# Kernel optimization log

Measured on AMD Instinct MI355X. Metric: run time of the kernel, lower is better.

Reference implementation:

```python
import jax, jax.numpy as jnp
import numpy as np

N, DF, DR, H, K = 4096, 128, 64, 1024, 10


def _init_linear(key, fan_in, fan_out):
    kw, kb = jax.random.split(key)
    bound = 1.0 / np.sqrt(fan_in)
    W = jax.random.uniform(kw, (fan_in, fan_out), jnp.float32, -bound, bound)
    b = jax.random.uniform(kb, (fan_out,), jnp.float32, -bound, bound)
    return W, b


def setup_inputs() -> dict:
    key = jax.random.key(0)
    ks = jax.random.split(key, 8)
    condition = jax.random.normal(ks[0], (N, DF), jnp.float32)
    tensor = jax.random.normal(ks[1], (N, DR), jnp.float32)
    Win, b_in = _init_linear(ks[2], DF + DR, H)
    W1, b1 = _init_linear(ks[3], H, H)
    W2, b2 = _init_linear(ks[4], H, H)
    W3, b3 = _init_linear(ks[5], H, H)
    Wout, b_out = _init_linear(ks[6], H, DR)
    return {"condition": condition, "tensor": tensor,
            "Win": Win, "b_in": b_in, "W1": W1, "b1": b1,
            "W2": W2, "b2": b2, "W3": W3, "b3": b3,
            "Wout": Wout, "b_out": b_out}


def _mlp(x, Win, b_in, W1, b1, W2, b2, W3, b3, Wout, b_out):
    # FFNN: input layer + 3 hidden layers with Softplus, linear output -> DR
    h = jax.nn.softplus(x @ Win + b_in)
    h = jax.nn.softplus(h @ W1 + b1)
    h = jax.nn.softplus(h @ W2 + b2)
    h = jax.nn.softplus(h @ W3 + b3)
    return h @ Wout + b_out


def reference(condition, tensor, Win, b_in, W1, b1, W2, b2, W3, b3, Wout, b_out):
    # torch.cdist(condition, condition), p=2 -> [N, N]
    sq = jnp.sum(condition * condition, axis=-1)
    d2 = sq[:, None] + sq[None, :] - 2.0 * (condition @ condition.T)
    dist = jnp.sqrt(jnp.maximum(d2, 0.0))
    # torch.topk(dist, 10, dim=1, largest=False) -> k nearest neighbor indices
    _, neighbor_idx = jax.lax.top_k(-dist, K)  # [N, K]
    # gather neighbor groups
    cond_g = condition[neighbor_idx]  # [N, K, DF]
    tens_g = tensor[neighbor_idx]     # [N, K, DR]
    # MongeMapNetwork.pushforward: tensor - MLP(concat(condition, tensor))
    x = jnp.concatenate([cond_g, tens_g], axis=-1)  # [N, K, DF+DR]
    pushed = tens_g - _mlp(x, Win, b_in, W1, b1, W2, b2, W3, b3, Wout, b_out)
    return pushed  # [N, K, DR]
```

## Files before the change

kernel.cpp:

```cpp
#include <hip/hip_runtime.h>
#include <hip/hip_fp16.h>
#include <stdint.h>

typedef unsigned short u16;
typedef unsigned int   u32;
typedef unsigned long long u64;
typedef short v8bf __attribute__((ext_vector_type(8)));
typedef float v4f  __attribute__((ext_vector_type(4)));
typedef u16   v8u  __attribute__((ext_vector_type(8)));

#define NPTS 4096
#define DF   128
#define DR   64
#define HID  1024
#define KNN  10
#define DIN  192

#define AS1 __attribute__((address_space(1)))
#define AS3 __attribute__((address_space(3)))

__device__ __forceinline__ float bf2f(u16 b){ return __uint_as_float(((unsigned)b)<<16); }
__device__ __forceinline__ u16 f2bf(float f){
  unsigned u = __float_as_uint(f);
  unsigned r = 0x7fffu + ((u>>16)&1u);
  return (u16)((u + r)>>16);
}
__device__ __forceinline__ u16 f2h(float f){
  __half h = __float2half(f);
  return __half_as_ushort(h);
}
__device__ __forceinline__ float softplus_f(float x){
  return x>15.f ? x : __logf(1.f + __expf(x));
}
__device__ __forceinline__ float rdv(const void* p, long j, int fl){
  return fl ? bf2f(((const u16*)p)[j]) : ((const float*)p)[j];
}
__device__ __forceinline__ void gl2lds16(const u16* g, u16* l){
  __builtin_amdgcn_global_load_lds((const AS1 unsigned int*)g, (AS3 unsigned int*)l, 16, 0, 0);
}

__global__ void detect_k(const u16* __restrict__ c, int* __restrict__ flag){
  __shared__ int cnt[256];
  int t = threadIdx.x, n = 0;
  for(int i=t; i<8192; i+=256){
    u16 v = c[2*i];
    int e = (v>>7)&0xff;
    n += (e>=96 && e<=158);
  }
  cnt[t] = n; __syncthreads();
  for(int s=128; s>0; s>>=1){ if(t<s) cnt[t]+=cnt[t+s]; __syncthreads(); }
  if(t==0) *flag = (cnt[0] > 4915) ? 1 : 0;
}

__global__ void prep_k(const void* cond, const void* tens,
    const void* Wi, const void* W1, const void* W2, const void* W3, const void* Wo,
    const void* bi, const void* b1, const void* b2, const void* b3, const void* bo,
    float* __restrict__ condF, float* __restrict__ tensF, float* __restrict__ biasF,
    u16* Oi, u16* O1, u16* O2, u16* O3, u16* Oo,
    float* __restrict__ sq, u16* __restrict__ X, const int* __restrict__ flag){
  __shared__ u16 tile[32][33];
  const int fl = *flag;
  const int bid = blockIdx.x, tid = threadIdx.x;
  if(bid < 3089){
    int i = bid*256 + tid;
    if(i < 524288){ condF[i] = rdv(cond, i, fl); }
    else if(i < 786432){ tensF[i-524288] = rdv(tens, i-524288, fl); }
    else{
      int j = i - 786432;
      if(j < 1024)      biasF[j] = rdv(bi, j, fl);
      else if(j < 2048) biasF[j] = rdv(b1, j-1024, fl);
      else if(j < 3072) biasF[j] = rdv(b2, j-2048, fl);
      else if(j < 4096) biasF[j] = rdv(b3, j-3072, fl);
      else if(j < 4160) biasF[j] = rdv(bo, j-4096, fl);
    }
  } else if(bid < 6417){
    int b = bid - 3089;
    const void* in; u16* out; int R, C, bx, by;
    if(b < 192)      {              in=Wi; out=Oi; R=192;  C=1024; bx=b&31; by=b>>5; }
    else if(b < 1216){ b -= 192;    in=W1; out=O1; R=1024; C=1024; bx=b&31; by=b>>5; }
    else if(b < 2240){ b -= 1216;   in=W2; out=O2; R=1024; C=1024; bx=b&31; by=b>>5; }
    else if(b < 3264){ b -= 2240;   in=W3; out=O3; R=1024; C=1024; bx=b&31; by=b>>5; }
    else             { b -= 3264;   in=Wo; out=Oo; R=1024; C=64;   bx=b&1;  by=b>>1; }
    int gx = bx*32, gy = by*32;
    int tx = tid&31, ty = tid>>5;
    #pragma unroll
    for(int r=ty; r<32; r+=8){
      size_t idx = (size_t)(gy+r)*C + gx + tx;
      tile[r][tx] = fl ? ((const u16*)in)[idx] : f2bf(((const float*)in)[idx]);
    }
    __syncthreads();
    #pragma unroll
    for(int r=ty; r<32; r+=8) out[(size_t)(gx+r)*R + gy + tx] = tile[tx][r];
  } else if(bid < 7441){
    int b = bid - 6417;
    int row = b*4 + (tid>>6), lane = tid&63;
    float a = rdv(cond, (long)row*DF + lane, fl);
    float c2 = rdv(cond, (long)row*DF + lane + 64, fl);
    double s = (double)a*a + (double)c2*c2;
    #pragma unroll
    for(int off=32; off>0; off>>=1) s += __shfl_down(s, off, 64);
    if(lane==0) sq[row] = (float)s;
  } else {
    int c = (bid-7441)*256 + tid;
    int j = c/48;
    int off = (c - j*48)*4;
    ushort4 o;
    if(off < DF){
      o.x = f2bf(rdv(cond, (long)j*DF + off + 0, fl));
      o.y = f2bf(rdv(cond, (long)j*DF + off + 1, fl));
      o.z = f2bf(rdv(cond, (long)j*DF + off + 2, fl));
      o.w = f2bf(rdv(cond, (long)j*DF + off + 3, fl));
    }else{
      int t2 = off - DF;
      o.x = f2bf(rdv(tens, (long)j*DR + t2 + 0, fl));
      o.y = f2bf(rdv(tens, (long)j*DR + t2 + 1, fl));
      o.z = f2bf(rdv(tens, (long)j*DR + t2 + 2, fl));
      o.w = f2bf(rdv(tens, (long)j*DR + t2 + 3, fl));
    }
    *(ushort4*)&X[(size_t)j*DIN + off] = o;
  }
}

__device__ __forceinline__ void gemm128_body(const u16* __restrict__ A,
    const u16* __restrict__ Bt, const float* __restrict__ bias, u16* __restrict__ C,
    int Kc, int bid, u16* As, u16* Bs){
  const int wg = (bid&7)*32 + (bid>>3);
  const int bm = (wg>>3)*128, bn = (wg&7)*128;
  const int lane = threadIdx.x&63, wave = threadIdx.x>>6;
  const int wm = (wave&1)*64, wn = (wave>>1)*64;
  const int sr = wave*32 + (lane>>2), sc = (lane&3)*8;
  const u16* pA0 = A  + (size_t)(bm+sr   )*Kc + sc;
  const u16* pA1 = A  + (size_t)(bm+sr+16)*Kc + sc;
  const u16* pB0 = Bt + (size_t)(bn+sr   )*Kc + sc;
  const u16* pB1 = Bt + (size_t)(bn+sr+16)*Kc + sc;
  u16* lA0 = &As[wave*1024];
  u16* lA1 = &As[wave*1024 + 512];
  u16* lB0 = &Bs[wave*1024];
  u16* lB1 = &Bs[wave*1024 + 512];
  const int m16 = lane&15, q = lane>>4;
  v4f acc[4][4] = {};
  for(int kb=0; kb<Kc; kb+=32){
    gl2lds16(pA0 + kb, lA0);
    gl2lds16(pA1 + kb, lA1);
    gl2lds16(pB0 + kb, lB0);
    gl2lds16(pB1 + kb, lB1);
    __syncthreads();
    v8bf a[4], b[4];
    #pragma unroll
    for(int x=0;x<4;x++){
      a[x] = *(const v8bf*)&As[(wm + x*16 + m16)*32 + q*8];
      b[x] = *(const v8bf*)&Bs[(wn + x*16 + m16)*32 + q*8];
    }
    #pragma unroll
    for(int mi=0;mi<4;mi++)
      #pragma unroll
      for(int ni=0;ni<4;ni++)
        acc[mi][ni] = __builtin_amdgcn_mfma_f32_16x16x32_bf16(a[mi], b[ni], acc[mi][ni], 0,0,0);
    __syncthreads();
  }
  const int col16 = lane&15, rowq = lane>>4;
  #pragma unroll
  for(int mi=0;mi<4;mi++){
    #pragma unroll
    for(int ni=0;ni<4;ni++){
      int cn = bn + wn + ni*16 + col16;
      float bi = bias[cn];
      #pragma unroll
      for(int r=0;r<4;r++){
        int rw = bm + wm + mi*16 + rowq*4 + r;
        float v = softplus_f(acc[mi][ni][r] + bi);
        C[(size_t)rw*HID + cn] = f2bf(v);
      }
    }
  }
}

__device__ __forceinline__ void knn_body(const u16* __restrict__ distH,
    const float* __restrict__ condF, int* __restrict__ nidx, int row,
    float* __restrict__ af, int* __restrict__ scnt,
    int* __restrict__ cand, u64* __restrict__ keys){
  const int lane = threadIdx.x&63;
  af[lane]    = condF[(size_t)row*DF + lane];
  af[lane+64] = condF[(size_t)row*DF + lane + 64];
  if(lane==0) *scnt = 0;
  const v8u* drow = (const v8u*)(distH + (size_t)row*NPTS);
  v8u vals[8];
  #pragma unroll
  for(int k=0;k<8;k++) vals[k] = drow[lane + k*64];
  u32 mx = 0;
  #pragma unroll
  for(int k=0;k<8;k++)
    #pragma unroll
    for(int e=0;e<8;e++){ u32 v = vals[k][e]; mx = v>mx ? v : mx; }
  #pragma unroll
  for(int off=32; off>0; off>>=1){
    u32 o = (u32)__shfl_down((int)mx, off, 64); mx = o>mx ? o : mx;
  }
  mx = (u32)__shfl((int)mx, 0, 64);
  u32 hi = mx+1, lo = 0;
  for(int it=0; it<17; ++it){
    u32 mid = (lo+hi)>>1;
    int c = 0;
    #pragma unroll
    for(int k=0;k<8;k++)
      #pragma unroll
      for(int e=0;e<8;e++) c += ((u32)vals[k][e] < mid);
    #pragma unroll
    for(int off=32; off>0; off>>=1) c += __shfl_down(c, off, 64);
    c = __shfl(c, 0, 64);
    if(c >= 16){ hi = mid; if(c <= 48) break; }
    else lo = mid;
  }
  const u32 t = hi;
  #pragma unroll
  for(int k=0;k<8;k++)
    #pragma unroll
    for(int e=0;e<8;e++){
      if((u32)vals[k][e] < t){
        int s = atomicAdd(scnt, 1);
        if(s < 64) cand[s] = (lane + k*64)*8 + e;
      }
    }
  int cnt = *scnt; if(cnt > 64) cnt = 64;
  u64 mykey = ~0ULL; int myj = -1;
  if(lane < cnt){
    int j = cand[lane];
    const float4* bp4 = (const float4*)(condF + (size_t)j*DF);
    double s = 0.0;
    #pragma unroll
    for(int v4i=0; v4i<32; v4i++){
      float4 bv = bp4[v4i];
      double d0 = (double)af[v4i*4+0]-(double)bv.x;
      double d1 = (double)af[v4i*4+1]-(double)bv.y;
      double d2 = (double)af[v4i*4+2]-(double)bv.z;
      double d3 = (double)af[v4i*4+3]-(double)bv.w;
      s += d0*d0 + d1*d1 + d2*d2 + d3*d3;
    }
    u64 bits = (u64)__double_as_longlong(s);
    mykey = (bits & ~0xFFFULL) | (u32)j;
    myj = j;
  }
  keys[lane] = mykey;
  if(lane < cnt){
    int rank = 0;
    for(int c2=0;c2<cnt;c2++) rank += (keys[c2] < mykey);
    if(rank < KNN) nidx[row*KNN + rank] = myj;
  }
}

__global__ __launch_bounds__(256,2) void gram_g1_k(const u16* __restrict__ condB,
    const float* __restrict__ condF, const float* __restrict__ sq,
    u16* __restrict__ distH, const int* __restrict__ flag,
    const u16* __restrict__ X, const u16* __restrict__ Wt_in,
    const float* __restrict__ biasF, u16* __restrict__ A0){
  __shared__ __align__(16) u16 smem[20480];
  const int bid = blockIdx.x;
  if(bid < 256){
    gemm128_body(X, Wt_in, biasF, A0, DIN, bid, smem, smem+4096);
    return;
  }
  const int gb = bid - 256;
  u16* Ahi = smem;
  u16* Alo = smem + 5120;
  u16* Bhi = smem + 10240;
  u16* Blo = smem + 15360;
  const int fl = *flag;
  const int bm = (gb&31)*128, bn = (gb>>5)*128;
  const int tid = threadIdx.x, lane = tid&63, wave = tid>>6;
  const int wm = (wave&1)*64, wn = (wave>>1)*64;
  v4f acc[4][4] = {};
  for(int kb=0; kb<DF; kb+=32){
    if(fl){
      #pragma unroll
      for(int t=0;t<2;t++){
        int c2 = tid + t*256;
        int r = c2>>2, col = (c2&3)*8;
        *(uint4*)&Ahi[r*40+col] = *(const uint4*)&condB[(size_t)(bm+r)*DF + kb + col];
        *(uint4*)&Bhi[r*40+col] = *(const uint4*)&condB[(size_t)(bn+r)*DF + kb + col];
      }
    }else{
      #pragma unroll
      for(int t=0;t<4;t++){
        int ch = tid + t*256;
        int r = ch>>3, c = (ch&7)*4;
        float4 av = *(const float4*)&condF[(size_t)(bm+r)*DF + kb + c];
        float4 bv = *(const float4*)&condF[(size_t)(bn+r)*DF + kb + c];
        ushort4 ah, bh, al, bl;
        ah.x=f2bf(av.x); ah.y=f2bf(av.y); ah.z=f2bf(av.z); ah.w=f2bf(av.w);
        bh.x=f2bf(bv.x); bh.y=f2bf(bv.y); bh.z=f2bf(bv.z); bh.w=f2bf(bv.w);
        al.x=f2bf(av.x-bf2f(ah.x)); al.y=f2bf(av.y-bf2f(ah.y));
        al.z=f2bf(av.z-bf2f(ah.z)); al.w=f2bf(av.w-bf2f(ah.w));
        bl.x=f2bf(bv.x-bf2f(bh.x)); bl.y=f2bf(bv.y-bf2f(bh.y));
        bl.z=f2bf(bv.z-bf2f(bh.z)); bl.w=f2bf(bv.w-bf2f(bh.w));
        *(ushort4*)&Ahi[r*40+c] = ah; *(ushort4*)&Bhi[r*40+c] = bh;
        *(ushort4*)&Alo[r*40+c] = al; *(ushort4*)&Blo[r*40+c] = bl;
      }
    }
    __syncthreads();
    const int m16 = lane&15, q = lane>>4;
    v8bf ahf[4], bhf[4];
    #pragma unroll
    for(int x=0;x<4;x++){
      ahf[x] = *(const v8bf*)&Ahi[(wm + x*16 + m16)*40 + q*8];
      bhf[x] = *(const v8bf*)&Bhi[(wn + x*16 + m16)*40 + q*8];
    }
    if(!fl){
      v8bf alf[4], blf[4];
      #pragma unroll
      for(int x=0;x<4;x++){
        alf[x] = *(const v8bf*)&Alo[(wm + x*16 + m16)*40 + q*8];
        blf[x] = *(const v8bf*)&Blo[(wn + x*16 + m16)*40 + q*8];
      }
      #pragma unroll
      for(int mi=0;mi<4;mi++)
        #pragma unroll
        for(int ni=0;ni<4;ni++){
          acc[mi][ni] = __builtin_amdgcn_mfma_f32_16x16x32_bf16(alf[mi], bhf[ni], acc[mi][ni], 0,0,0);
          acc[mi][ni] = __builtin_amdgcn_mfma_f32_16x16x32_bf16(ahf[mi], blf[ni], acc[mi][ni], 0,0,0);
        }
    }
    #pragma unroll
    for(int mi=0;mi<4;mi++)
      #pragma unroll
      for(int ni=0;ni<4;ni++)
        acc[mi][ni] = __builtin_amdgcn_mfma_f32_16x16x32_bf16(ahf[mi], bhf[ni], acc[mi][ni], 0,0,0);
    __syncthreads();
  }
  const int col16 = lane&15, rowq = lane>>4;
  #pragma unroll
  for(int mi=0;mi<4;mi++){
    #pragma unroll
    for(int ni=0;ni<4;ni++){
      int cj = bn + wn + ni*16 + col16;
      float sqj = sq[cj];
      #pragma unroll
      for(int r=0;r<4;r++){
        int ri = bm + wm + mi*16 + rowq*4 + r;
        float d2 = (sq[ri] + sqj) - 2.0f*acc[mi][ni][r];
        distH[(size_t)ri*NPTS + cj] = f2h(fmaxf(d2, 0.f));
      }
    }
  }
}

__global__ __launch_bounds__(256,2) void gemm_knn_k(const u16* __restrict__ A,
    const u16* __restrict__ Bt, const float* __restrict__ bias, u16* __restrict__ C,
    const u16* __restrict__ distH, const float* __restrict__ condF,
    int* __restrict__ nidx, int rowoff){
  __shared__ __align__(16) u16 gsm[8192];
  __shared__ float af[4][DF];
  __shared__ int   scnt[4];
  __shared__ int   cand[4][64];
  __shared__ u64   keys[4][64];
  const int bid = blockIdx.x;
  if(bid < 256){
    gemm128_body(A, Bt, bias, C, HID, bid, gsm, gsm+4096);
  } else {
    const int wv = threadIdx.x>>6;
    const int row = rowoff + (bid-256)*4 + wv;
    knn_body(distH, condF, nidx, row, af[wv], &scnt[wv], cand[wv], keys[wv]);
  }
}

__global__ __launch_bounds__(256,2) void gemm_bt_k(const u16* __restrict__ A,
    const u16* __restrict__ Bt, const float* __restrict__ bias, u16* __restrict__ C){
  __shared__ __align__(16) u16 As[4096];
  __shared__ __align__(16) u16 Bs[4096];
  gemm128_body(A, Bt, bias, C, HID, blockIdx.x, As, Bs);
}

__global__ __launch_bounds__(256,2) void gemm_out_k(const u16* __restrict__ A,
    const u16* __restrict__ Bt, float* __restrict__ Pp){
  __shared__ __align__(16) u16 As[128*32];
  __shared__ __align__(16) u16 Bs[64*32];
  const int bm = (blockIdx.x>>2)*128;
  const int k0 = (blockIdx.x&3)*256;
  float* P = Pp + (size_t)(blockIdx.x&3)*262144;
  const int tid = threadIdx.x, lane = tid&63, wave = tid>>6;
  const int wm = wave*32;
  int c0 = wave*128 + lane, c1 = c0 + 64;
  int ra0 = c0>>2, qa0 = c0&3, ra1 = c1>>2, qa1 = c1&3;
  int cb = wave*64 + lane;
  int rb = cb>>2, qb = cb&3;
  const u16* pA0 = A  + (size_t)(bm+ra0)*HID + qa0*8;
  const u16* pA1 = A  + (size_t)(bm+ra1)*HID + qa1*8;
  const u16* pB  = Bt + (size_t)rb*HID + qb*8;
  u16* lA0 = &As[(wave*128     )*8];
  u16* lA1 = &As[(wave*128 + 64)*8];
  u16* lB  = &Bs[(wave*64      )*8];
  const int m16 = lane&15, q = lane>>4;
  v4f acc[2][4] = {};
  for(int kb=k0; kb<k0+256; kb+=32){
    gl2lds16(pA0 + kb, lA0);
    gl2lds16(pA1 + kb, lA1);
    gl2lds16(pB  + kb, lB);
    __syncthreads();
    v8bf a[2], b[4];
    a[0] = *(const v8bf*)&As[(wm + m16)*32 + q*8];
    a[1] = *(const v8bf*)&As[(wm + 16 + m16)*32 + q*8];
    #pragma unroll
    for(int x=0;x<4;x++) b[x] = *(const v8bf*)&Bs[(x*16 + m16)*32 + q*8];
    #pragma unroll
    for(int mi=0;mi<2;mi++)
      #pragma unroll
      for(int ni=0;ni<4;ni++)
        acc[mi][ni] = __builtin_amdgcn_mfma_f32_16x16x32_bf16(a[mi], b[ni], acc[mi][ni], 0,0,0);
    __syncthreads();
  }
  const int col16 = lane&15, rowq = lane>>4;
  #pragma unroll
  for(int mi=0;mi<2;mi++){
    #pragma unroll
    for(int ni=0;ni<4;ni++){
      int cn = ni*16 + col16;
      #pragma unroll
      for(int r=0;r<4;r++){
        int rw = bm + wm + mi*16 + rowq*4 + r;
        P[(size_t)rw*DR + cn] = acc[mi][ni][r];
      }
    }
  }
}

__global__ void gather_k(const float* __restrict__ Pp, const float* __restrict__ tensF,
                         const float* __restrict__ biasF, const int* __restrict__ nidx,
                         void* __restrict__ outv, const int* __restrict__ flag){
  const int fl = *flag;
  int e = blockIdx.x*256 + threadIdx.x;
  int m = e>>4;
  int c = (e&15)*4;
  int j = nidx[m] & (NPTS-1);
  size_t rc = (size_t)j*DR + c;
  float4 t  = *(const float4*)&tensF[rc];
  float4 b  = *(const float4*)&biasF[4096 + c];
  float4 p0 = *(const float4*)&Pp[rc];
  float4 p1 = *(const float4*)&Pp[262144 + rc];
  float4 p2 = *(const float4*)&Pp[524288 + rc];
  float4 p3 = *(const float4*)&Pp[786432 + rc];
  float4 v;
  v.x = t.x - (b.x + ((p0.x+p1.x)+(p2.x+p3.x)));
  v.y = t.y - (b.y + ((p0.y+p1.y)+(p2.y+p3.y)));
  v.z = t.z - (b.z + ((p0.z+p1.z)+(p2.z+p3.z)));
  v.w = t.w - (b.w + ((p0.w+p1.w)+(p2.w+p3.w)));
  if(fl){
    ushort4 o; o.x=f2bf(v.x); o.y=f2bf(v.y); o.z=f2bf(v.z); o.w=f2bf(v.w);
    *(ushort4*)&((u16*)outv)[(size_t)m*DR + c] = o;
  }else{
    *(float4*)&((float*)outv)[(size_t)m*DR + c] = v;
  }
}

constexpr size_t OFF_FLAG  = 0;
constexpr size_t OFF_SQ    = 256;
constexpr size_t OFF_NIDX  = OFF_SQ    + 16384;
constexpr size_t OFF_BIAS  = OFF_NIDX  + 163840;
constexpr size_t OFF_CONDF = OFF_BIAS  + 16640;
constexpr size_t OFF_TENSF = OFF_CONDF + 2097152;
constexpr size_t OFF_WTIN  = OFF_TENSF + 1048576;
constexpr size_t OFF_WT1   = OFF_WTIN  + 393216;
constexpr size_t OFF_WT2   = OFF_WT1   + 2097152;
constexpr size_t OFF_WT3   = OFF_WT2   + 2097152;
constexpr size_t OFF_WTO   = OFF_WT3   + 2097152;
constexpr size_t OFF_DIST  = OFF_WTO   + 131072;
constexpr size_t OFF_X     = OFF_DIST  + 33554432;
constexpr size_t OFF_A0    = OFF_X     + 1572864;
constexpr size_t OFF_A1    = OFF_A0    + 8388608;
constexpr size_t OFF_P     = OFF_A1    + 8388608;

extern "C" void kernel_launch(void* const* d_in, const int* in_sizes, int n_in,
                              void* d_out, int out_size, void* d_ws, size_t ws_size,
                              hipStream_t stream){
  char* ws = (char*)d_ws;
  int*   flag  = (int*)  (ws + OFF_FLAG);
  float* sqv   = (float*)(ws + OFF_SQ);
  int*   nidx  = (int*)  (ws + OFF_NIDX);
  float* biasF = (float*)(ws + OFF_BIAS);
  float* condF = (float*)(ws + OFF_CONDF);
  float* tensF = (float*)(ws + OFF_TENSF);
  u16*   Wt_in = (u16*)  (ws + OFF_WTIN);
  u16*   Wt1   = (u16*)  (ws + OFF_WT1);
  u16*   Wt2   = (u16*)  (ws + OFF_WT2);
  u16*   Wt3   = (u16*)  (ws + OFF_WT3);
  u16*   Wt_o  = (u16*)  (ws + OFF_WTO);
  u16*   distH = (u16*)  (ws + OFF_DIST);
  u16*   X     = (u16*)  (ws + OFF_X);
  u16*   A0    = (u16*)  (ws + OFF_A0);
  u16*   A1    = (u16*)  (ws + OFF_A1);
  float* Pp    = (float*)(ws + OFF_P);

  detect_k <<<1, 256, 0, stream>>>((const u16*)d_in[0], flag);
  prep_k   <<<8209, 256, 0, stream>>>(d_in[0], d_in[1],
                d_in[2], d_in[4], d_in[6], d_in[8], d_in[10],
                d_in[3], d_in[5], d_in[7], d_in[9], d_in[11],
                condF, tensF, biasF, Wt_in, Wt1, Wt2, Wt3, Wt_o, sqv, X, flag);
  gram_g1_k<<<1280, 256, 0, stream>>>((const u16*)d_in[0], condF, sqv, distH, flag,
                                      X, Wt_in, biasF, A0);
  gemm_knn_k<<<768, 256, 0, stream>>>(A0, Wt1, biasF+1024, A1, distH, condF, nidx, 0);
  gemm_knn_k<<<768, 256, 0, stream>>>(A1, Wt2, biasF+2048, A0, distH, condF, nidx, 2048);
  gemm_bt_k  <<<256, 256, 0, stream>>>(A0, Wt3, biasF+3072, A1);
  gemm_out_k <<<128, 256, 0, stream>>>(A1, Wt_o, Pp);
  gather_k   <<<2560, 256, 0, stream>>>(Pp, tensF, biasF, nidx, d_out, flag);
}
```

Before: 221.5 us.

## Switch MLP GEMMs to 128x64 tiles with 64-deep K steps

Reworks the shared GEMM body from 128x128 output tiles with a 32-wide K step to 128x64 tiles that load two 32-wide K slices per barrier pair. This doubles the GEMM workgroup count from 256 to 512, giving better occupancy across the CUs on a 4096x1024 problem, and halves the number of sync points per K. The block-to-tile mapping is also changed so that each XCD covers contiguous row blocks, aiming at L2 locality. In exchange, the smaller N tile lowers per-block operand reuse and raises the total A-tile reloads.

```diff
diff --git a/kernel.cpp b/kernel.cpp
--- a/kernel.cpp
+++ b/kernel.cpp
@@ -121,55 +121,60 @@
   }
 }
 
-__device__ __forceinline__ void gemm128_body(const u16* __restrict__ A,
+__device__ __forceinline__ void gemm_bt_body(const u16* __restrict__ A,
     const u16* __restrict__ Bt, const float* __restrict__ bias, u16* __restrict__ C,
-    int Kc, int bid, u16* As, u16* Bs){
-  const int wg = (bid&7)*32 + (bid>>3);
-  const int bm = (wg>>3)*128, bn = (wg&7)*128;
-  const int lane = threadIdx.x&63, wave = threadIdx.x>>6;
-  const int wm = (wave&1)*64, wn = (wave>>1)*64;
-  const int sr = wave*32 + (lane>>2), sc = (lane&3)*8;
-  const u16* pA0 = A  + (size_t)(bm+sr   )*Kc + sc;
-  const u16* pA1 = A  + (size_t)(bm+sr+16)*Kc + sc;
-  const u16* pB0 = Bt + (size_t)(bn+sr   )*Kc + sc;
-  const u16* pB1 = Bt + (size_t)(bn+sr+16)*Kc + sc;
+    int Nc, int Kc, int bid, u16* As, u16* Bs){
+  const int xcd = bid&7, slot = bid>>3;
+  const int bm = (xcd*4 + (slot>>4)) * 128;
+  const int bn = (slot&15) * 64;
+  const int tid = threadIdx.x, lane = tid&63, wave = tid>>6;
+  const int wm = (wave&1)*64, wn = (wave>>1)*32;
+  int c0 = wave*128 + lane, c1 = c0 + 64;
+  int r0 = c0>>2, q0 = c0&3, r1 = c1>>2, q1 = c1&3;
+  int cb = wave*64 + lane, rb = cb>>2, qb = cb&3;
+  const u16* pA0 = A  + (size_t)(bm+r0)*Kc + q0*8;
+  const u16* pA1 = A  + (size_t)(bm+r1)*Kc + q1*8;
+  const u16* pB  = Bt + (size_t)(bn+rb)*Kc + qb*8;
   u16* lA0 = &As[wave*1024];
   u16* lA1 = &As[wave*1024 + 512];
-  u16* lB0 = &Bs[wave*1024];
-  u16* lB1 = &Bs[wave*1024 + 512];
+  u16* lB  = &Bs[wave*512];
   const int m16 = lane&15, q = lane>>4;
-  v4f acc[4][4] = {};
-  for(int kb=0; kb<Kc; kb+=32){
+  v4f acc[4][2] = {};
+  for(int kb=0; kb<Kc; kb+=64){
     gl2lds16(pA0 + kb, lA0);
     gl2lds16(pA1 + kb, lA1);
-    gl2lds16(pB0 + kb, lB0);
-    gl2lds16(pB1 + kb, lB1);
-    __syncthreads();
-    v8bf a[4], b[4];
-    #pragma unroll
-    for(int x=0;x<4;x++){
-      a[x] = *(const v8bf*)&As[(wm + x*16 + m16)*32 + q*8];
-      b[x] = *(const v8bf*)&Bs[(wn + x*16 + m16)*32 + q*8];
-    }
-    #pragma unroll
-    for(int mi=0;mi<4;mi++)
-      #pragma unroll
-      for(int ni=0;ni<4;ni++)
-        acc[mi][ni] = __builtin_amdgcn_mfma_f32_16x16x32_bf16(a[mi], b[ni], acc[mi][ni], 0,0,0);
+    gl2lds16(pB  + kb, lB);
+    gl2lds16(pA0 + kb + 32, lA0 + 4096);
+    gl2lds16(pA1 + kb + 32, lA1 + 4096);
+    gl2lds16(pB  + kb + 32, lB + 2048);
+    __syncthreads();
+    #pragma unroll
+    for(int kk=0;kk<2;kk++){
+      v8bf a[4], b[2];
+      #pragma unroll
+      for(int x=0;x<4;x++) a[x] = *(const v8bf*)&As[kk*4096 + (wm + x*16 + m16)*32 + q*8];
+      #pragma unroll
+      for(int x=0;x<2;x++) b[x] = *(const v8bf*)&Bs[kk*2048 + (wn + x*16 + m16)*32 + q*8];
+      #pragma unroll
+      for(int mi=0;mi<4;mi++)
+        #pragma unroll
+        for(int ni=0;ni<2;ni++)
+          acc[mi][ni] = __builtin_amdgcn_mfma_f32_16x16x32_bf16(a[mi], b[ni], acc[mi][ni], 0,0,0);
+    }
     __syncthreads();
   }
   const int col16 = lane&15, rowq = lane>>4;
   #pragma unroll
   for(int mi=0;mi<4;mi++){
     #pragma unroll
-    for(int ni=0;ni<4;ni++){
+    for(int ni=0;ni<2;ni++){
       int cn = bn + wn + ni*16 + col16;
       float bi = bias[cn];
       #pragma unroll
       for(int r=0;r<4;r++){
         int rw = bm + wm + mi*16 + rowq*4 + r;
         float v = softplus_f(acc[mi][ni][r] + bi);
-        C[(size_t)rw*HID + cn] = f2bf(v);
+        C[(size_t)rw*Nc + cn] = f2bf(v);
       }
     }
   }
@@ -255,11 +260,11 @@
     const float* __restrict__ biasF, u16* __restrict__ A0){
   __shared__ __align__(16) u16 smem[20480];
   const int bid = blockIdx.x;
-  if(bid < 256){
-    gemm128_body(X, Wt_in, biasF, A0, DIN, bid, smem, smem+4096);
+  if(bid < 512){
+    gemm_bt_body(X, Wt_in, biasF, A0, HID, DIN, bid, smem, smem+8192);
     return;
   }
-  const int gb = bid - 256;
+  const int gb = bid - 512;
   u16* Ahi = smem;
   u16* Alo = smem + 5120;
   u16* Bhi = smem + 10240;
@@ -347,26 +352,26 @@
     const u16* __restrict__ Bt, const float* __restrict__ bias, u16* __restrict__ C,
     const u16* __restrict__ distH, const float* __restrict__ condF,
     int* __restrict__ nidx, int rowoff){
-  __shared__ __align__(16) u16 gsm[8192];
+  __shared__ __align__(16) u16 gsm[12288];
   __shared__ float af[4][DF];
   __shared__ int   scnt[4];
   __shared__ int   cand[4][64];
   __shared__ u64   keys[4][64];
   const int bid = blockIdx.x;
-  if(bid < 256){
-    gemm128_body(A, Bt, bias, C, HID, bid, gsm, gsm+4096);
+  if(bid < 512){
+    gemm_bt_body(A, Bt, bias, C, HID, HID, bid, gsm, gsm+8192);
   } else {
     const int wv = threadIdx.x>>6;
-    const int row = rowoff + (bid-256)*4 + wv;
+    const int row = rowoff + (bid-512)*4 + wv;
     knn_body(distH, condF, nidx, row, af[wv], &scnt[wv], cand[wv], keys[wv]);
   }
 }
 
 __global__ __launch_bounds__(256,2) void gemm_bt_k(const u16* __restrict__ A,
     const u16* __restrict__ Bt, const float* __restrict__ bias, u16* __restrict__ C){
-  __shared__ __align__(16) u16 As[4096];
+  __shared__ __align__(16) u16 As[8192];
   __shared__ __align__(16) u16 Bs[4096];
-  gemm128_body(A, Bt, bias, C, HID, blockIdx.x, As, Bs);
+  gemm_bt_body(A, Bt, bias, C, HID, HID, blockIdx.x, As, Bs);
 }
 
 __global__ __launch_bounds__(256,2) void gemm_out_k(const u16* __restrict__ A,
@@ -493,11 +498,11 @@
                 d_in[2], d_in[4], d_in[6], d_in[8], d_in[10],
                 d_in[3], d_in[5], d_in[7], d_in[9], d_in[11],
                 condF, tensF, biasF, Wt_in, Wt1, Wt2, Wt3, Wt_o, sqv, X, flag);
-  gram_g1_k<<<1280, 256, 0, stream>>>((const u16*)d_in[0], condF, sqv, distH, flag,
+  gram_g1_k<<<1536, 256, 0, stream>>>((const u16*)d_in[0], condF, sqv, distH, flag,
                                       X, Wt_in, biasF, A0);
-  gemm_knn_k<<<768, 256, 0, stream>>>(A0, Wt1, biasF+1024, A1, distH, condF, nidx, 0);
-  gemm_knn_k<<<768, 256, 0, stream>>>(A1, Wt2, biasF+2048, A0, distH, condF, nidx, 2048);
-  gemm_bt_k  <<<256, 256, 0, stream>>>(A0, Wt3, biasF+3072, A1);
+  gemm_knn_k<<<1024, 256, 0, stream>>>(A0, Wt1, biasF+1024, A1, distH, condF, nidx, 0);
+  gemm_knn_k<<<1024, 256, 0, stream>>>(A1, Wt2, biasF+2048, A0, distH, condF, nidx, 2048);
+  gemm_bt_k  <<<512, 256, 0, stream>>>(A0, Wt3, biasF+3072, A1);
   gemm_out_k <<<128, 256, 0, stream>>>(A1, Wt_o, Pp);
   gather_k   <<<2560, 256, 0, stream>>>(Pp, tensF, biasF, nidx, d_out, flag);
 }
```

New measurement: 209.6 us. 5.4% less time.
